# Kernel tuning notes

Hardware: AMD Instinct MI355X
Metric: run time of the kernel (lower is better)

## Reference

```python
import jax, jax.numpy as jnp
import numpy as np

D_MODEL = 1024

def setup_inputs() -> dict:
    key = jax.random.key(0)
    ks = jax.random.split(key, 7)
    scale = 1.0 / np.sqrt(D_MODEL)
    x = jax.random.normal(ks[0], (4, 2048, D_MODEL), dtype=jnp.float32)
    # nn.Linear weights are [out, in]; init uniform(-1/sqrt(in), 1/sqrt(in))
    wq = jax.random.uniform(ks[1], (D_MODEL, D_MODEL), jnp.float32, -scale, scale)
    wk = jax.random.uniform(ks[2], (D_MODEL, D_MODEL), jnp.float32, -scale, scale)
    wv = jax.random.uniform(ks[3], (D_MODEL, D_MODEL), jnp.float32, -scale, scale)
    bq = jax.random.uniform(ks[4], (D_MODEL,), jnp.float32, -scale, scale)
    bk = jax.random.uniform(ks[5], (D_MODEL,), jnp.float32, -scale, scale)
    bv = jax.random.uniform(ks[6], (D_MODEL,), jnp.float32, -scale, scale)
    return {"x": x, "wq": wq, "bq": bq, "wk": wk, "bk": bk, "wv": wv, "bv": bv}

def reference(x, wq, bq, wk, bk, wv, bv):
    B, T, C = x.shape
    q = jnp.einsum('btc,dc->btd', x, wq) + bq  # Linear: x @ W^T + b
    k = jnp.einsum('btc,dc->btd', x, wk) + bk
    v = jnp.einsum('btc,dc->btd', x, wv) + bv
    scores = jnp.einsum('bqd,bkd->bqk', q, k) / jnp.sqrt(jnp.float32(C))
    causal = jnp.tril(jnp.ones((T, T), dtype=bool))  # True = keep
    scores = jnp.where(causal, scores, jnp.finfo(scores.dtype).min)
    attn = jax.nn.softmax(scores, axis=-1)
    return jnp.einsum('bqk,bkd->bqd', attn, v)
```

## Files before the change

kernel.cpp:

```cpp
#include <hip/hip_runtime.h>
#include <math.h>

#define BATCH 4
#define SEQ   2048
#define DM    1024
#define NTOK  (BATCH * SEQ)

typedef __attribute__((ext_vector_type(8))) short bf16x8;
typedef __attribute__((ext_vector_type(4))) float f32x4;
typedef unsigned short u16;
struct alignas(8) us4 { u16 x, y, z, w; };

__device__ __forceinline__ u16 f2bf(float f) {
    union { float f; unsigned u; } v; v.f = f;
    unsigned r = v.u + 0x7fffu + ((v.u >> 16) & 1u);
    return (u16)(r >> 16);
}

__device__ __forceinline__ void gload_lds16(const void* g, void* l) {
    __builtin_amdgcn_global_load_lds(
        (const __attribute__((address_space(1))) unsigned int*)g,
        (__attribute__((address_space(3))) unsigned int*)l, 16, 0, 0);
}

#define VM0 asm volatile("s_waitcnt vmcnt(0)" ::: "memory")
#define BAR __builtin_amdgcn_s_barrier()

__device__ __forceinline__ bf16x8 ldsF(const u16* T, int fr, int kk, int lane)
{
    const int row  = fr * 16 + (lane & 15);
    const int colb = (kk * 64 + ((lane >> 4) << 4)) ^ ((row & 7) << 4);
    return *(const bf16x8*)(T + row * 64 + (colb >> 1));
}


__device__ __forceinline__ void stageH(const u16* __restrict__ G, int ld,
    int row0, int kt, u16* half_lds, int wid, int lane)
{
    #pragma unroll
    for (int j = 0; j < 2; ++j) {
        const int base = j * 8192 + wid * 1024;
        const int off  = base + lane * 16;
        const int row  = off >> 7;
        const int colb = (off & 127) ^ ((row & 7) << 4);
        gload_lds16(G + (size_t)(row0 + row) * ld + kt + (colb >> 1),
                    (char*)half_lds + base);
    }
}

template<int MB, int NB>
__device__ __forceinline__ void mma16(const bf16x8 A[4][2], const bf16x8 B[2][2],
                                      f32x4 acc[8][4])
{
    __builtin_amdgcn_s_setprio(1);
    #pragma unroll
    for (int i = 0; i < 4; ++i)
        #pragma unroll
        for (int j = 0; j < 2; ++j)
            #pragma unroll
            for (int kk = 0; kk < 2; ++kk)
                acc[MB + i][NB + j] = __builtin_amdgcn_mfma_f32_16x16x32_bf16(
                    A[i][kk], B[j][kk], acc[MB + i][NB + j], 0, 0, 0);
    __builtin_amdgcn_s_setprio(0);
}

__global__ __launch_bounds__(512, 2) void qkv_mfma8(
    const u16* __restrict__ xb,
    const u16* __restrict__ wqb, const float* __restrict__ bq,
    const u16* __restrict__ wkb, const float* __restrict__ bk,
    const u16* __restrict__ wvb, const float* __restrict__ bv,
    u16* __restrict__ qb, u16* __restrict__ kb, u16* __restrict__ vT)
{
    __shared__ alignas(16) u16 LDS[65536];
    const int z = blockIdx.z;
    const u16* W = (z == 0) ? wqb : (z == 1) ? wkb : wvb;
    const float* bias = (z == 0) ? bq : (z == 1) ? bk : bv;
    const int m0 = blockIdx.x * 256, n0 = blockIdx.y * 256;
    const int t = threadIdx.x, wid = t >> 6, lane = t & 63;
    const int wm = wid >> 2, wn = wid & 3;

    f32x4 acc[8][4] = {};

    stageH(xb, DM, m0,       0, LDS + 0,            wid, lane);
    stageH(xb, DM, m0 + 128, 0, LDS + 8192,         wid, lane);
    stageH(W,  DM, n0,       0, LDS + 32768,        wid, lane);
    stageH(W,  DM, n0 + 128, 0, LDS + 32768 + 8192, wid, lane);
    VM0;
    BAR;

    bf16x8 rA0[4][2], rA1[4][2], rB[2][2];

    #pragma unroll 1
    for (int ti = 0; ti < 16; ++ti) {
        const int cur = ti & 1, nxt = cur ^ 1;
        u16* Ac0 = LDS + cur * 16384;
        u16* Ac1 = Ac0 + 8192;
        u16* Bc0 = LDS + 32768 + cur * 16384;
        u16* Bc1 = Bc0 + 8192;
        u16* An0 = LDS + nxt * 16384;
        u16* An1 = An0 + 8192;
        u16* Bn0 = LDS + 32768 + nxt * 16384;
        u16* Bn1 = Bn0 + 8192;
        const int kt1 = (ti + 1) * 64;
        const bool st = ti < 15;

        #pragma unroll
        for (int i = 0; i < 4; ++i) {
            rA0[i][0] = ldsF(Ac0, 2 * i + wm, 0, lane);
            rA0[i][1] = ldsF(Ac0, 2 * i + wm, 1, lane);
        }
        #pragma unroll
        for (int j = 0; j < 2; ++j) {
            rB[j][0] = ldsF(Bc0, 4 * j + wn, 0, lane);
            rB[j][1] = ldsF(Bc0, 4 * j + wn, 1, lane);
        }
        if (st) {
            stageH(xb, DM, m0,       kt1, An0, wid, lane);
            stageH(W,  DM, n0,       kt1, Bn0, wid, lane);
        }
        mma16<0, 0>(rA0, rB, acc);

        #pragma unroll
        for (int i = 0; i < 4; ++i) {
            rA1[i][0] = ldsF(Ac1, 2 * i + wm, 0, lane);
            rA1[i][1] = ldsF(Ac1, 2 * i + wm, 1, lane);
        }
        if (st) stageH(xb, DM, m0 + 128, kt1, An1, wid, lane);
        mma16<4, 0>(rA1, rB, acc);

        #pragma unroll
        for (int j = 0; j < 2; ++j) {
            rB[j][0] = ldsF(Bc1, 4 * j + wn, 0, lane);
            rB[j][1] = ldsF(Bc1, 4 * j + wn, 1, lane);
        }
        if (st) stageH(W, DM, n0 + 128, kt1, Bn1, wid, lane);
        mma16<4, 2>(rA1, rB, acc);

        mma16<0, 2>(rA0, rB, acc);

        VM0;
        BAR;
    }

    const int lrow = lane & 15, lhi = lane >> 4;
    if (z < 2) {
        u16* outp = (z == 0) ? qb : kb;
        #pragma unroll
        for (int nf = 0; nf < 4; ++nf) {
            const int n = n0 + (4 * nf + wn) * 16 + lrow;
            const float bn = bias[n];
            #pragma unroll
            for (int mf = 0; mf < 8; ++mf) {
                const int mb = m0 + (2 * mf + wm) * 16 + lhi * 4;
                #pragma unroll
                for (int r = 0; r < 4; ++r)
                    outp[(size_t)(mb + r) * DM + n] = f2bf(acc[mf][nf][r] + bn);
            }
        }
    } else {
        #pragma unroll
        for (int nf = 0; nf < 4; ++nf) {
            const int nloc = nf * 16 + lrow;
            const int n = n0 + (4 * nf + wn) * 16 + lrow;
            const float bn = bias[n];
            #pragma unroll
            for (int mf = 0; mf < 8; ++mf) {
                const int mloc0 = (2 * mf + wm) * 16 + lhi * 4;
                const int idx = (wn * 16384 + nloc * 256 + mloc0)
                                ^ ((nloc & 7) << 3);
                us4 p{f2bf(acc[mf][nf][0] + bn), f2bf(acc[mf][nf][1] + bn),
                      f2bf(acc[mf][nf][2] + bn), f2bf(acc[mf][nf][3] + bn)};
                *(us4*)(LDS + idx) = p;
            }
        }
        BAR;
        const int c = t & 31;
        #pragma unroll 1
        for (int rr = t >> 5; rr < 256; rr += 16) {
            const int lr2 = rr & 15, wn2 = (rr >> 4) & 3, nf2 = rr >> 6;
            const int nloc = nf2 * 16 + lr2;
            const int idx = (wn2 * 16384 + nloc * 256 + c * 8)
                            ^ ((nloc & 7) << 3);
            bf16x8 v = *(const bf16x8*)(LDS + idx);
            *(bf16x8*)(vT + (size_t)(n0 + rr) * NTOK + m0 + c * 8) = v;
        }
    }
}


__device__ __forceinline__ void stage64(const u16* __restrict__ G, int ld,
    int row0, int kt, u16* lds, int wid, int lane)
{
    #pragma unroll
    for (int j = 0; j < 4; ++j) {
        const int base = j * 4096 + wid * 1024;
        const int off  = base + lane * 16;
        const int row  = off >> 7;
        const int colb = (off & 127) ^ ((row & 7) << 4);
        gload_lds16(G + (size_t)(row0 + row) * ld + kt + (colb >> 1),
                    (char*)lds + base);
    }
}

__device__ __forceinline__ void frag_mma64(
    const u16* As, const u16* Bs, int wr, int wc, int lane, f32x4 acc[4][4])
{
    #pragma unroll
    for (int kk = 0; kk < 2; ++kk) {
        bf16x8 a[4], b[4];
        #pragma unroll
        for (int i = 0; i < 4; ++i) a[i] = ldsF(As, wr * 4 + i, kk, lane);
        #pragma unroll
        for (int j = 0; j < 4; ++j) b[j] = ldsF(Bs, wc * 4 + j, kk, lane);
        #pragma unroll
        for (int i = 0; i < 4; ++i)
            #pragma unroll
            for (int j = 0; j < 4; ++j)
                acc[i][j] = __builtin_amdgcn_mfma_f32_16x16x32_bf16(
                    a[i], b[j], acc[i][j], 0, 0, 0);
    }
}

__global__ __launch_bounds__(256) void conv_flat(
    const float* __restrict__ x,
    const float* __restrict__ w0, const float* __restrict__ w1,
    const float* __restrict__ w2,
    u16* __restrict__ xo,
    u16* __restrict__ o0, u16* __restrict__ o1, u16* __restrict__ o2)
{
    const int X4  = NTOK * DM / 4;
    const int W4  = DM * DM / 4;
    const int TOT = X4 + 3 * W4;
    for (int i = blockIdx.x * 256 + threadIdx.x; i < TOT; i += gridDim.x * 256) {
        const float* in; u16* out; int idx;
        if (i < X4) { in = x; out = xo; idx = i; }
        else {
            const int j = i - X4, s = j >> 18;
            idx = j & (W4 - 1);
            in  = (s == 0) ? w0 : (s == 1) ? w1 : w2;
            out = (s == 0) ? o0 : (s == 1) ? o1 : o2;
        }
        float4 f = ((const float4*)in)[idx];
        us4 p{f2bf(f.x), f2bf(f.y), f2bf(f.z), f2bf(f.w)};
        ((us4*)out)[idx] = p;
    }
}

__global__ __launch_bounds__(256, 3) void qk_exp(
    const u16* __restrict__ qb, const u16* __restrict__ kb,
    u16* __restrict__ attn, float* __restrict__ psum)
{
    const int m0 = blockIdx.x * 128, n0 = blockIdx.y * 128;
    if (n0 > m0) return;
    __shared__ u16 As[128 * 64], Bs[128 * 64];
    const int b = blockIdx.z;
    const u16* A = qb + (size_t)b * SEQ * DM;
    const u16* B = kb + (size_t)b * SEQ * DM;
    u16* P = attn + (size_t)b * SEQ * SEQ;
    const int t = threadIdx.x, wid = t >> 6, lane = t & 63;
    const int wr = wid >> 1, wc = wid & 1;

    f32x4 acc[4][4] = {};
    for (int kt = 0; kt < DM; kt += 64) {
        __syncthreads();
        stage64(A, DM, m0, kt, As, wid, lane);
        stage64(B, DM, n0, kt, Bs, wid, lane);
        __syncthreads();
        frag_mma64(As, Bs, wr, wc, lane, acc);
    }
    const int lrow = lane & 15, lg = lane >> 4;
    const float scale = 0.03125f;
    const int nb = (n0 >> 6) | wc;
    #pragma unroll
    for (int mi = 0; mi < 4; ++mi) {
        #pragma unroll
        for (int r = 0; r < 4; ++r) {
            const int row = m0 + wr * 64 + mi * 16 + lg * 4 + r;
            float ps = 0.f;
            #pragma unroll
            for (int ni = 0; ni < 4; ++ni) {
                const int n = n0 + wc * 64 + ni * 16 + lrow;
                const float p = (n <= row) ? __expf(acc[mi][ni][r] * scale) : 0.f;
                P[(size_t)row * SEQ + n] = f2bf(p);
                ps += p;
            }
            #pragma unroll
            for (int mk = 1; mk < 16; mk <<= 1) ps += __shfl_xor(ps, mk);
            if (lrow == 0)
                psum[((size_t)b * SEQ + row) * 32 + nb] = ps;
        }
    }
}

__global__ __launch_bounds__(256, 3) void pv_mfma(
    const u16* __restrict__ attn, const u16* __restrict__ vT,
    const float* __restrict__ psum, float* __restrict__ out)
{
    __shared__ u16 As[128 * 64], Bs[128 * 64];
    __shared__ float invs[128];
    const int bid = blockIdx.x;
    const int xcd = bid & 7, rdec = bid >> 3;
    const int n0i = rdec & 7, ghi = rdec >> 3;
    const int g = ghi * 8 + xcd;
    const int m0 = (g & 15) * 128, n0 = n0i * 128;
    const int b = g >> 4;
    const u16* A = attn + (size_t)b * SEQ * SEQ;
    const u16* B = vT + (size_t)b * SEQ;
    float* C = out + (size_t)b * SEQ * DM;
    const int t = threadIdx.x, wid = t >> 6, lane = t & 63;
    const int wr = wid >> 1, wc = wid & 1;

    if (t < 128) {
        const int row = m0 + t;
        const float* pr = psum + ((size_t)b * SEQ + row) * 32;
        const int nbmax = (row >> 6) | 1;
        float s = 0.f;
        for (int nbi = 0; nbi <= nbmax; ++nbi) s += pr[nbi];
        invs[t] = 1.f / s;
    }

    f32x4 acc[4][4] = {};
    const int kmax = m0 + 128;
    for (int kt = 0; kt < kmax; kt += 64) {
        __syncthreads();
        stage64(A, SEQ,  m0, kt, As, wid, lane);
        stage64(B, NTOK, n0, kt, Bs, wid, lane);
        __syncthreads();
        frag_mma64(As, Bs, wr, wc, lane, acc);
    }
    const int lrow = lane & 15, lg = lane >> 4;
    #pragma unroll
    for (int mi = 0; mi < 4; ++mi) {
        const int ml = wr * 64 + mi * 16 + lg * 4;
        #pragma unroll
        for (int ni = 0; ni < 4; ++ni) {
            const int n = n0 + wc * 64 + ni * 16 + lrow;
            #pragma unroll
            for (int r = 0; r < 4; ++r)
                C[(size_t)(m0 + ml + r) * DM + n] = acc[mi][ni][r] * invs[ml + r];
        }
    }
}

extern "C" void kernel_launch(void* const* d_in, const int* in_sizes, int n_in,
                              void* d_out, int out_size, void* d_ws, size_t ws_size,
                              hipStream_t stream)
{
    const float* x  = (const float*)d_in[0];
    const float* wq = (const float*)d_in[1];
    const float* bq = (const float*)d_in[2];
    const float* wk = (const float*)d_in[3];
    const float* bk = (const float*)d_in[4];
    const float* wv = (const float*)d_in[5];
    const float* bv = (const float*)d_in[6];
    float* out = (float*)d_out;

    u16* ws  = (u16*)d_ws;
    u16* xb  = ws;
    u16* wqb = xb  + (size_t)NTOK * DM;
    u16* wkb = wqb + (size_t)DM * DM;
    u16* wvb = wkb + (size_t)DM * DM;
    u16* qb  = wvb + (size_t)DM * DM;
    u16* kb  = qb  + (size_t)NTOK * DM;
    u16* vT  = kb  + (size_t)NTOK * DM;
    u16* attn = vT + (size_t)NTOK * DM;
    float* psum = (float*)(attn + (size_t)BATCH * SEQ * SEQ);

    conv_flat<<<2048, 256, 0, stream>>>(
        x, wq, wk, wv, xb, wqb, wkb, wvb);

    qkv_mfma8<<<dim3(NTOK / 256, DM / 256, 3), 512, 0, stream>>>(
        xb, wqb, bq, wkb, bk, wvb, bv, qb, kb, vT);

    qk_exp<<<dim3(SEQ / 128, SEQ / 128, BATCH), 256, 0, stream>>>(
        qb, kb, attn, psum);

    pv_mfma<<<512, 256, 0, stream>>>(attn, vT, psum, out);
}
```

Baseline: 146.5 us.

## Stage Q/K epilogue through LDS for coalesced stores; launch only causal tiles

```diff
diff --git a/kernel.cpp b/kernel.cpp
--- a/kernel.cpp
+++ b/kernel.cpp
@@ -147,15 +147,27 @@
         u16* outp = (z == 0) ? qb : kb;
         #pragma unroll
         for (int nf = 0; nf < 4; ++nf) {
-            const int n = n0 + (4 * nf + wn) * 16 + lrow;
-            const float bn = bias[n];
+            const int nloc = (4 * nf + wn) * 16 + lrow;
+            const float bn = bias[n0 + nloc];
             #pragma unroll
             for (int mf = 0; mf < 8; ++mf) {
-                const int mb = m0 + (2 * mf + wm) * 16 + lhi * 4;
+                const int mloc0 = (2 * mf + wm) * 16 + lhi * 4;
                 #pragma unroll
-                for (int r = 0; r < 4; ++r)
-                    outp[(size_t)(mb + r) * DM + n] = f2bf(acc[mf][nf][r] + bn);
+                for (int r = 0; r < 4; ++r) {
+                    const int mloc = mloc0 + r;
+                    const int bidx = (mloc * 512 + nloc * 2)
+                                     ^ ((mloc & 7) << 4);
+                    *(u16*)((char*)LDS + bidx) = f2bf(acc[mf][nf][r] + bn);
+                }
             }
+        }
+        BAR;
+        const int c = t & 31;
+        #pragma unroll 1
+        for (int rr = t >> 5; rr < 256; rr += 16) {
+            const int bidx = rr * 512 + ((c * 16) ^ ((rr & 7) << 4));
+            bf16x8 v = *(const bf16x8*)((char*)LDS + bidx);
+            *(bf16x8*)(outp + (size_t)(m0 + rr) * DM + n0 + c * 8) = v;
         }
     } else {
         #pragma unroll
@@ -250,8 +262,9 @@
     const u16* __restrict__ qb, const u16* __restrict__ kb,
     u16* __restrict__ attn, float* __restrict__ psum)
 {
-    const int m0 = blockIdx.x * 128, n0 = blockIdx.y * 128;
-    if (n0 > m0) return;
+    int ti = blockIdx.x, mi = 0;
+    while (ti >= mi + 1) { ti -= mi + 1; ++mi; }
+    const int m0 = mi * 128, n0 = ti * 128;
     __shared__ u16 As[128 * 64], Bs[128 * 64];
     const int b = blockIdx.z;
     const u16* A = qb + (size_t)b * SEQ * DM;
@@ -272,15 +285,15 @@
     const float scale = 0.03125f;
     const int nb = (n0 >> 6) | wc;
     #pragma unroll
-    for (int mi = 0; mi < 4; ++mi) {
+    for (int mi2 = 0; mi2 < 4; ++mi2) {
         #pragma unroll
         for (int r = 0; r < 4; ++r) {
-            const int row = m0 + wr * 64 + mi * 16 + lg * 4 + r;
+            const int row = m0 + wr * 64 + mi2 * 16 + lg * 4 + r;
             float ps = 0.f;
             #pragma unroll
             for (int ni = 0; ni < 4; ++ni) {
                 const int n = n0 + wc * 64 + ni * 16 + lrow;
-                const float p = (n <= row) ? __expf(acc[mi][ni][r] * scale) : 0.f;
+                const float p = (n <= row) ? __expf(acc[mi2][ni][r] * scale) : 0.f;
                 P[(size_t)row * SEQ + n] = f2bf(p);
                 ps += p;
             }
@@ -372,8 +385,7 @@
     qkv_mfma8<<<dim3(NTOK / 256, DM / 256, 3), 512, 0, stream>>>(
         xb, wqb, bq, wkb, bk, wvb, bv, qb, kb, vT);
 
-    qk_exp<<<dim3(SEQ / 128, SEQ / 128, BATCH), 256, 0, stream>>>(
-        qb, kb, attn, psum);
+    qk_exp<<<dim3(136, 1, BATCH), 256, 0, stream>>>(qb, kb, attn, psum);
 
     pv_mfma<<<512, 256, 0, stream>>>(attn, vT, psum, out);
 }
```

After: 153.8 us. +5.0%, slower.
